# Kernel optimization log

Hardware: AMD Instinct MI355X
Metric: run time of the kernel (lower is better)

## Reference

```python
import jax, jax.numpy as jnp
import numpy as np

# matcher cost weights (init_kwargs)
W_CLASS, W_3DCENTER, W_BBOX, W_GIOU = 2.0, 10.0, 5.0, 2.0
ALPHA, GAMMA, EPS = 0.25, 2.0, 1e-8


def _box_cxcylrtb_to_xyxy(b):
    # (cx, cy, l, r, t, b) -> (x1, y1, x2, y2)
    cx, cy, l, r, t, bo = (b[..., i] for i in range(6))
    return jnp.stack([cx - l, cy - t, cx + r, cy + bo], axis=-1)


def _generalized_box_iou(b1, b2):
    # b1 [N,4], b2 [M,4] in xyxy -> GIoU matrix [N,M]
    area1 = (b1[:, 2] - b1[:, 0]) * (b1[:, 3] - b1[:, 1])
    area2 = (b2[:, 2] - b2[:, 0]) * (b2[:, 3] - b2[:, 1])
    lt = jnp.maximum(b1[:, None, :2], b2[None, :, :2])
    rb = jnp.minimum(b1[:, None, 2:], b2[None, :, 2:])
    wh = jnp.clip(rb - lt, 0.0)
    inter = wh[..., 0] * wh[..., 1]
    union = area1[:, None] + area2[None, :] - inter
    iou = inter / union
    lt_e = jnp.minimum(b1[:, None, :2], b2[None, :, :2])
    rb_e = jnp.maximum(b1[:, None, 2:], b2[None, :, 2:])
    wh_e = jnp.clip(rb_e - lt_e, 0.0)
    area_e = wh_e[..., 0] * wh_e[..., 1]
    return iou - (area_e - union) / area_e


def _l1_cdist(a, b):
    return jnp.abs(a[:, None, :] - b[None, :, :]).sum(-1)


def _cost_matrix(pred_logits, pred_boxes, tgt_labels, tgt_boxes):
    bs, nq, _ = pred_boxes.shape
    out_prob = jax.nn.sigmoid(pred_logits.reshape(bs * nq, -1))
    tgt_ids = tgt_labels.reshape(-1)
    neg = (1.0 - ALPHA) * out_prob ** GAMMA * -jnp.log(1.0 - out_prob + EPS)
    pos = ALPHA * (1.0 - out_prob) ** GAMMA * -jnp.log(out_prob + EPS)
    cost_class = (pos - neg)[:, tgt_ids]              # [bs*nq, bs*nt]
    out_flat = pred_boxes.reshape(bs * nq, 6)
    tgt_flat = tgt_boxes.reshape(-1, 6)
    cost_3dcenter = _l1_cdist(out_flat[:, 0:2], tgt_flat[:, 0:2])
    cost_bbox = _l1_cdist(out_flat[:, 2:6], tgt_flat[:, 2:6])
    cost_giou = -_generalized_box_iou(_box_cxcylrtb_to_xyxy(out_flat), _box_cxcylrtb_to_xyxy(tgt_flat))
    C = W_BBOX * cost_bbox + W_3DCENTER * cost_3dcenter + W_CLASS * cost_class + W_GIOU * cost_giou
    return C.reshape(bs, nq, -1)


def _lsa(cost):
    # Rectangular linear sum assignment (Jonker-Volgenant / e-maxx Hungarian),
    # scipy.optimize.linear_sum_assignment compatible (row-sorted output).
    cost = np.asarray(cost, dtype=np.float64)
    transposed = cost.shape[0] > cost.shape[1]
    if transposed:
        cost = cost.T
    n, m = cost.shape  # n <= m
    u = np.zeros(n + 1)
    v = np.zeros(m + 1)
    p = np.zeros(m + 1, dtype=np.int64)    # p[j] = row matched to col j (1-indexed)
    way = np.zeros(m + 1, dtype=np.int64)
    INF = np.inf
    for i in range(1, n + 1):
        p[0] = i
        j0 = 0
        minv = np.full(m + 1, INF)
        used = np.zeros(m + 1, dtype=bool)
        while True:
            used[j0] = True
            i0 = p[j0]
            free = ~used[1:]
            cur = cost[i0 - 1, :] - u[i0] - v[1:]
            upd = free & (cur < minv[1:])
            minv[1:][upd] = cur[upd]
            way[1:][upd] = j0
            cand = np.where(free, minv[1:], INF)
            j1 = int(np.argmin(cand)) + 1
            delta = cand[j1 - 1]
            u[p[used]] += delta
            v[used] -= delta
            minv[~used] -= delta
            j0 = j1
            if p[j0] == 0:
                break
        while j0 != 0:
            j1 = way[j0]
            p[j0] = p[j1]
            j0 = j1
    cols = np.nonzero(p[1:])[0]
    rows = p[1:][cols] - 1
    if transposed:
        rows, cols = cols, rows
    order = np.argsort(rows)
    return rows[order], cols[order]


def _assign(Cn, nt, group_num):
    # per-sample block-diagonal cost slicing + per-group Hungarian, like the torch loop
    bs, nq, _ = Cn.shape
    g_nq = nq // group_num
    pred_idx, tgt_idx = [], []
    for b in range(bs):
        Cb = Cn[b, :, b * nt:(b + 1) * nt]
        rows, cols = [], []
        for g in range(group_num):
            r, c = _lsa(Cb[g * g_nq:(g + 1) * g_nq])
            rows.append(r + g * g_nq)
            cols.append(c)
        pred_idx.append(np.concatenate(rows))
        tgt_idx.append(np.concatenate(cols))
    return np.stack(pred_idx), np.stack(tgt_idx)


def setup_inputs() -> dict:
    key = jax.random.key(0)
    k1, k2, k3, k4 = jax.random.split(key, 4)
    bs, nq, nc, nt = 16, 550, 91, 48
    return {
        "pred_logits": jax.random.normal(k1, (bs, nq, nc), jnp.float32),
        "pred_boxes": jax.random.uniform(k2, (bs, nq, 6), jnp.float32),
        "tgt_labels": jax.random.randint(k3, (bs, nt), 0, nc),
        "tgt_boxes": jax.random.uniform(k4, (bs, nt, 6), jnp.float32),
        "group_num": 11,
    }


def reference(pred_logits, pred_boxes, tgt_labels, tgt_boxes, group_num):
    C = _cost_matrix(pred_logits, pred_boxes, tgt_labels, tgt_boxes)  # [bs, nq, bs*nt]
    nt = tgt_boxes.shape[1]
    Cn = np.asarray(jax.device_get(C), dtype=np.float64)
    pi, ti = _assign(Cn, nt, int(group_num))
    return C, jnp.asarray(pi), jnp.asarray(ti)
```

## Files before the change

### kernel.cpp

```cpp
#include <hip/hip_runtime.h>
#include <math.h>

#define BS 16
#define NQ 550
#define NC 91
#define NT 48
#define GN 11
#define GQ 50
#define NTOT (BS * NT)
#define NROW 48
#define MCOL 50
#define NPAIR (GN * NT)
#define NLSA (BS * GN)

__device__ __forceinline__ float focal_cost_f32(float x) {
    float prob = 1.0f / (1.0f + __expf(-x));
    float q = 1.0f - prob;
    float lneg = __logf(q + 1e-8f);
    float lpos = __logf(prob + 1e-8f);
    float neg = 0.75f * (prob * prob) * (-lneg);
    float pos = 0.25f * (q * q) * (-lpos);
    return pos - neg;
}

__device__ __forceinline__ float cost_element(
    const float* __restrict__ logits,
    const float* __restrict__ pboxes, const int* __restrict__ labels,
    const float* __restrict__ tboxes, int p, int t)
{
    const float* pb = pboxes + (long)p * 6;
    float pcx = pb[0], pcy = pb[1], pl = pb[2], pr = pb[3], ptt = pb[4], pbo = pb[5];
    const float* tb = tboxes + (long)t * 6;
    float tcx = tb[0], tcy = tb[1], tl = tb[2], tr = tb[3], ttt = tb[4], tbo = tb[5];

    float c3d = __fadd_rn(fabsf(__fsub_rn(pcx, tcx)), fabsf(__fsub_rn(pcy, tcy)));
    float cbb = __fadd_rn(
                  __fadd_rn(
                    __fadd_rn(fabsf(__fsub_rn(pl, tl)), fabsf(__fsub_rn(pr, tr))),
                    fabsf(__fsub_rn(ptt, ttt))),
                  fabsf(__fsub_rn(pbo, tbo)));

    float px1 = __fsub_rn(pcx, pl), py1 = __fsub_rn(pcy, ptt);
    float px2 = __fadd_rn(pcx, pr), py2 = __fadd_rn(pcy, pbo);
    float tx1 = __fsub_rn(tcx, tl), ty1 = __fsub_rn(tcy, ttt);
    float tx2 = __fadd_rn(tcx, tr), ty2 = __fadd_rn(tcy, tbo);

    float area1 = __fmul_rn(__fsub_rn(px2, px1), __fsub_rn(py2, py1));
    float area2 = __fmul_rn(__fsub_rn(tx2, tx1), __fsub_rn(ty2, ty1));
    float ltx = fmaxf(px1, tx1), lty = fmaxf(py1, ty1);
    float rbx = fminf(px2, tx2), rby = fminf(py2, ty2);
    float wx = fmaxf(__fsub_rn(rbx, ltx), 0.0f);
    float wy = fmaxf(__fsub_rn(rby, lty), 0.0f);
    float inter = __fmul_rn(wx, wy);
    float uni = __fsub_rn(__fadd_rn(area1, area2), inter);
    float iou = __fdiv_rn(inter, uni);
    float ex1 = fminf(px1, tx1), ey1 = fminf(py1, ty1);
    float ex2 = fmaxf(px2, tx2), ey2 = fmaxf(py2, ty2);
    float ew = fmaxf(__fsub_rn(ex2, ex1), 0.0f);
    float eh = fmaxf(__fsub_rn(ey2, ey1), 0.0f);
    float earea = __fmul_rn(ew, eh);
    float giou = __fsub_rn(iou, __fdiv_rn(__fsub_rn(earea, uni), earea));
    float cgiou = -giou;

    float cclass = focal_cost_f32(logits[(long)p * NC + labels[t]]);

    float out = __fmul_rn(5.0f, cbb);
    out = __fadd_rn(out, __fmul_rn(10.0f, c3d));
    out = __fadd_rn(out, __fmul_rn(2.0f, cclass));
    out = __fadd_rn(out, __fmul_rn(2.0f, cgiou));
    return out;
}

__device__ __forceinline__ double readlane_f64(double x, int l) {
    long long b = __double_as_longlong(x);
    int lo = __builtin_amdgcn_readlane((int)(b & 0xffffffffLL), l);
    int hi = __builtin_amdgcn_readlane((int)(b >> 32), l);
    return __longlong_as_double(((long long)hi << 32) | (unsigned int)lo);
}

__device__ __forceinline__ unsigned fkey_u32(float f) {
    unsigned b = __float_as_uint(f);
    return b ^ (unsigned)(((int)b >> 31) | 0x80000000);
}

template <int CTRL>
__device__ __forceinline__ unsigned dpp_min_u32(unsigned x) {
    unsigned t = (unsigned)__builtin_amdgcn_update_dpp((int)x, (int)x, CTRL, 0xf, 0xf, false);
    return (x < t) ? x : t;
}

__global__ __launch_bounds__(256) void mega_kernel(
    const float* __restrict__ logits,
    const float* __restrict__ pboxes,
    const int*   __restrict__ labels,
    const float* __restrict__ tboxes,
    float*       __restrict__ C,
    float*       __restrict__ pi,
    float*       __restrict__ ti)
{
    if (blockIdx.x >= NLSA) {
        long idx = (long)(blockIdx.x - NLSA) * 256 + threadIdx.x;
        if (idx >= (long)BS * NQ * NTOT) return;
        int t = (int)(idx % NTOT);
        int p = (int)(idx / NTOT);
        C[idx] = cost_element(logits, pboxes, labels, tboxes, p, t);
        return;
    }

    const int blk = blockIdx.x;
    const int b = blk / GN, g = blk % GN;
    const int tid = threadIdx.x;

    __shared__ double lcost[NROW * MCOL];

    for (int k = tid; k < NROW * MCOL; k += 256) {
        int i = k % NROW, j = k / NROW;
        float cf = cost_element(logits, pboxes, labels, tboxes,
                                b * NQ + g * GQ + j, b * NT + i);
        lcost[i * MCOL + j] = (double)cf;
    }
    __syncthreads();
    if (tid >= 64) return;

    const int lane = tid;
    const bool incol = (lane >= 1 && lane <= MCOL);
    const int cidx = incol ? lane - 1 : 0;
    const double INF = __builtin_inf();
    const float INFF = __builtin_inff();

    int    pcol_l = 0;
    double urow_l = 0.0;
    double v_l    = 0.0;
    int    way_l  = 0;
    double minv_l = INF;
    float  kprev  = INFF;
    bool   used_l = false;

    for (int i = 1; i <= NROW; ++i) {
        if (lane == 0) { pcol_l = i; urow_l = 0.0; }
        minv_l = INF;
        kprev  = INFF;
        used_l = false;
        int j0 = 0;
        int i0 = i;
        double u_i0 = 0.0;
        double cd = lcost[(i0 - 1) * MCOL + cidx];

        for (int guard = 0; guard <= MCOL + 1; ++guard) {
            used_l = used_l || (lane == j0);
            bool freel = incol && !used_l;

            double cur = (cd - u_i0) - v_l;
            bool upd   = freel && (cur < minv_l);
            minv_l = upd ? cur : minv_l;
            way_l  = upd ? j0  : way_l;

            float kf = freel ? fminf(__double2float_rn(cur), kprev) : INFF;

            unsigned ukey = fkey_u32(kf);
            unsigned red = ukey;
            red = dpp_min_u32<0x111>(red);
            red = dpp_min_u32<0x112>(red);
            red = dpp_min_u32<0x114>(red);
            red = dpp_min_u32<0x118>(red);
            unsigned m0 = (unsigned)__builtin_amdgcn_readlane((int)red, 15);
            unsigned m1 = (unsigned)__builtin_amdgcn_readlane((int)red, 31);
            unsigned m2 = (unsigned)__builtin_amdgcn_readlane((int)red, 47);
            unsigned m3 = (unsigned)__builtin_amdgcn_readlane((int)red, 63);
            unsigned ka = (m0 < m1) ? m0 : m1;
            unsigned kb = (m2 < m3) ? m2 : m3;
            unsigned kmin = (ka < kb) ? ka : kb;

            unsigned long long mm = __ballot(ukey == kmin);
            int j1 = (int)__builtin_ctzll(mm);

            int    i0n   = __builtin_amdgcn_readlane(pcol_l, j1);
            double delta = readlane_f64(minv_l, j1);
            double u_nx  = readlane_f64(urow_l, j1);

            int r_next = (i0n > 0) ? (i0n - 1) : 0;
            double cd_next = lcost[r_next * MCOL + cidx];

            urow_l = used_l ? urow_l + delta : urow_l;
            v_l    = used_l ? v_l - delta    : v_l;
            minv_l = freel  ? minv_l - delta : minv_l;
            kprev  = __double2float_rn(minv_l);

            j0 = j1;
            if (i0n == 0) break;
            i0   = i0n;
            u_i0 = u_nx;
            cd   = cd_next;
        }

        int j = j0;
        while (j != 0) {
            int wj    = __builtin_amdgcn_readlane(way_l, j);
            int pr    = __builtin_amdgcn_readlane(pcol_l, wj);
            double ur = readlane_f64(urow_l, wj);
            if (lane == j) { pcol_l = pr; urow_l = ur; }
            j = wj;
        }
    }

    unsigned long long asg = __ballot(incol && pcol_l != 0);
    if (incol && pcol_l != 0) {
        int k = __popcll(asg & ((1ull << lane) - 1));
        float* pib = pi + ((long)b * NPAIR + (long)g * NT);
        float* tib = ti + ((long)b * NPAIR + (long)g * NT);
        pib[k] = (float)(g * GQ + cidx);
        tib[k] = (float)(pcol_l - 1);
    }
}

extern "C" void kernel_launch(void* const* d_in, const int* in_sizes, int n_in,
                              void* d_out, int out_size, void* d_ws, size_t ws_size,
                              hipStream_t stream) {
    const float* logits = (const float*)d_in[0];
    const float* pboxes = (const float*)d_in[1];
    const int*   labels = (const int*)d_in[2];
    const float* tboxes = (const float*)d_in[3];

    float* out = (float*)d_out;
    float* C  = out;
    float* pi = out + (long)BS * NQ * NTOT;
    float* ti = pi + (long)BS * NPAIR;

    long total = (long)BS * NQ * NTOT;
    int cost_blocks = (int)((total + 255) / 256);
    int mega_blocks = NLSA + cost_blocks;

    mega_kernel<<<mega_blocks, 256, 0, stream>>>(
        logits, pboxes, labels, tboxes, C, pi, ti);
}
```

Before: 160.4 us.

## Speculatively prefetch next Hungarian row cost from LDS before argmin resolves

```diff
diff --git a/kernel.cpp b/kernel.cpp
--- a/kernel.cpp
+++ b/kernel.cpp
@@ -89,6 +89,22 @@
     return (x < t) ? x : t;
 }
 
+#define WAVE_MIN_U32(ukey, kmin_out)                                          \
+    {                                                                         \
+        unsigned red_ = (ukey);                                               \
+        red_ = dpp_min_u32<0x111>(red_);                                      \
+        red_ = dpp_min_u32<0x112>(red_);                                      \
+        red_ = dpp_min_u32<0x114>(red_);                                      \
+        red_ = dpp_min_u32<0x118>(red_);                                      \
+        unsigned a_ = (unsigned)__builtin_amdgcn_readlane((int)red_, 15);     \
+        unsigned b_ = (unsigned)__builtin_amdgcn_readlane((int)red_, 31);     \
+        unsigned c_ = (unsigned)__builtin_amdgcn_readlane((int)red_, 47);     \
+        unsigned d_ = (unsigned)__builtin_amdgcn_readlane((int)red_, 63);     \
+        unsigned e_ = (a_ < b_) ? a_ : b_;                                    \
+        unsigned f_ = (c_ < d_) ? c_ : d_;                                    \
+        (kmin_out) = (e_ < f_) ? e_ : f_;                                     \
+    }
+
 __global__ __launch_bounds__(256) void mega_kernel(
     const float* __restrict__ logits,
     const float* __restrict__ pboxes,
@@ -136,6 +152,8 @@
     float  kprev  = INFF;
     bool   used_l = false;
 
+    double cd_phase = lcost[0 * MCOL + cidx];
+
     for (int i = 1; i <= NROW; ++i) {
         if (lane == 0) { pcol_l = i; urow_l = 0.0; }
         minv_l = INF;
@@ -144,7 +162,10 @@
         int j0 = 0;
         int i0 = i;
         double u_i0 = 0.0;
-        double cd = lcost[(i0 - 1) * MCOL + cidx];
+        double cd = cd_phase;
+
+        int    spec_row = -1;
+        double spec_val = 0.0;
 
         for (int guard = 0; guard <= MCOL + 1; ++guard) {
             used_l = used_l || (lane == j0);
@@ -156,35 +177,47 @@
             way_l  = upd ? j0  : way_l;
 
             float kf = freel ? fminf(__double2float_rn(cur), kprev) : INFF;
-
             unsigned ukey = fkey_u32(kf);
-            unsigned red = ukey;
-            red = dpp_min_u32<0x111>(red);
-            red = dpp_min_u32<0x112>(red);
-            red = dpp_min_u32<0x114>(red);
-            red = dpp_min_u32<0x118>(red);
-            unsigned m0 = (unsigned)__builtin_amdgcn_readlane((int)red, 15);
-            unsigned m1 = (unsigned)__builtin_amdgcn_readlane((int)red, 31);
-            unsigned m2 = (unsigned)__builtin_amdgcn_readlane((int)red, 47);
-            unsigned m3 = (unsigned)__builtin_amdgcn_readlane((int)red, 63);
-            unsigned ka = (m0 < m1) ? m0 : m1;
-            unsigned kb = (m2 < m3) ? m2 : m3;
-            unsigned kmin = (ka < kb) ? ka : kb;
+            unsigned kmin;
+            WAVE_MIN_U32(ukey, kmin);
 
             unsigned long long mm = __ballot(ukey == kmin);
             int j1 = (int)__builtin_ctzll(mm);
 
-            int    i0n   = __builtin_amdgcn_readlane(pcol_l, j1);
+            int i0n = __builtin_amdgcn_readlane(pcol_l, j1);
+
+            int r_true = (i0n > 0) ? (i0n - 1) : 0;
+            double cd_next;
+            if (i0n > 0 && r_true == spec_row) {
+                cd_next = spec_val;
+            } else {
+                cd_next = lcost[r_true * MCOL + cidx];
+            }
+
             double delta = readlane_f64(minv_l, j1);
             double u_nx  = readlane_f64(urow_l, j1);
-
-            int r_next = (i0n > 0) ? (i0n - 1) : 0;
-            double cd_next = lcost[r_next * MCOL + cidx];
 
             urow_l = used_l ? urow_l + delta : urow_l;
             v_l    = used_l ? v_l - delta    : v_l;
             minv_l = freel  ? minv_l - delta : minv_l;
             kprev  = __double2float_rn(minv_l);
+
+            {
+                unsigned us = (freel && lane != j1) ? fkey_u32(kprev)
+                                                    : 0xFFFFFFFFu;
+                unsigned skmin;
+                WAVE_MIN_U32(us, skmin);
+                unsigned long long smm = __ballot(us == skmin);
+                spec_row = -1;
+                if (smm != 0ull) {
+                    int sj = (int)__builtin_ctzll(smm);
+                    int sp = __builtin_amdgcn_readlane(pcol_l, sj);
+                    if (sp > 0) {
+                        spec_row = sp - 1;
+                        spec_val = lcost[spec_row * MCOL + cidx];
+                    }
+                }
+            }
 
             j0 = j1;
             if (i0n == 0) break;
@@ -192,6 +225,8 @@
             u_i0 = u_nx;
             cd   = cd_next;
         }
+
+        if (i < NROW) cd_phase = lcost[i * MCOL + cidx];
 
         int j = j0;
         while (j != 0) {
```

Measured after the change: 216.4 us. 35.0% more time.
